# Kernel optimization log

Measured on AMD Instinct MI355X. Metric: run time of the kernel, lower is better.

Reference implementation:

```python
import jax, jax.numpy as jnp
import numpy as np

D_MODEL = 512; N_HEADS = 8; HEAD = D_MODEL // N_HEADS; D_FF = 2048
N_LAYERS = 4; VOCAB = 32000; B = 2; S = 1024; T = 1024


def _posenc(seq_len, d_model):
    pos = np.arange(seq_len)[:, None].astype(np.float32)
    div = np.exp(np.arange(0, d_model, 2).astype(np.float32) * (-np.log(10000.0) / d_model))
    pe = np.zeros((seq_len, d_model), dtype=np.float32)
    pe[:, 0::2] = np.sin(pos * div)
    pe[:, 1::2] = np.cos(pos * div)
    return jnp.asarray(pe)


def _layernorm(x, g, b, eps=1e-6):
    mean = x.mean(-1, keepdims=True)
    xc = x - mean
    # torch .var() is unbiased (ddof=1) -- replicate exactly
    var = (xc * xc).sum(-1, keepdims=True) / (x.shape[-1] - 1)
    return g * (xc * (var + eps) ** -0.5) + b


def _mha(q, k, v, w, mask):
    # w: [4, D, D] stacked (W_q, W_k, W_v, W_o), applied as x @ W
    def heads(x, wi):
        return (x @ wi).reshape(x.shape[0], x.shape[1], N_HEADS, HEAD).transpose(0, 2, 1, 3)
    Q, K, V = heads(q, w[0]), heads(k, w[1]), heads(v, w[2])  # [B,H,S,hd]
    att = jnp.einsum('bhqd,bhkd->bhqk', Q, K) * HEAD ** (-0.5)
    att = jnp.where(mask == 0, -jnp.inf, att)
    att = jax.nn.softmax(att, axis=-1)
    y = jnp.einsum('bhqk,bhkd->bhqd', att, V)
    y = y.transpose(0, 2, 1, 3).reshape(q.shape[0], q.shape[1], D_MODEL)
    return y @ w[3]


def _ff(x, w1, b1, w2, b2):
    return jax.nn.relu(x @ w1 + b1) @ w2 + b2


def setup_inputs() -> dict:
    key = jax.random.key(0)
    ks = iter(jax.random.split(key, 32))
    std = 0.02
    inp = {}
    inp['src'] = jax.random.randint(next(ks), (B, S), 0, VOCAB)
    inp['tgt'] = jax.random.randint(next(ks), (B, T), 0, VOCAB)
    inp['src_mask'] = jnp.ones((B, 1, 1, S), dtype=jnp.int32)
    inp['tgt_mask'] = jnp.tril(jnp.ones((T, T), dtype=jnp.int32))[None, None].repeat(B, axis=0)
    inp['src_emb'] = jax.random.normal(next(ks), (VOCAB, D_MODEL)) * std
    inp['tgt_emb'] = jax.random.normal(next(ks), (VOCAB, D_MODEL)) * std
    inp['enc_att_w'] = jax.random.normal(next(ks), (N_LAYERS, 4, D_MODEL, D_MODEL)) * std
    inp['enc_ff_w1'] = jax.random.normal(next(ks), (N_LAYERS, D_MODEL, D_FF)) * std
    inp['enc_ff_b1'] = jnp.zeros((N_LAYERS, D_FF))
    inp['enc_ff_w2'] = jax.random.normal(next(ks), (N_LAYERS, D_FF, D_MODEL)) * std
    inp['enc_ff_b2'] = jnp.zeros((N_LAYERS, D_MODEL))
    inp['enc_norm_g'] = jnp.ones((N_LAYERS, 2, D_MODEL))
    inp['enc_norm_b'] = jnp.zeros((N_LAYERS, 2, D_MODEL))
    inp['enc_final_g'] = jnp.ones((D_MODEL,))
    inp['enc_final_b'] = jnp.zeros((D_MODEL,))
    inp['dec_att_w'] = jax.random.normal(next(ks), (N_LAYERS, 2, 4, D_MODEL, D_MODEL)) * std
    inp['dec_ff_w1'] = jax.random.normal(next(ks), (N_LAYERS, D_MODEL, D_FF)) * std
    inp['dec_ff_b1'] = jnp.zeros((N_LAYERS, D_FF))
    inp['dec_ff_w2'] = jax.random.normal(next(ks), (N_LAYERS, D_FF, D_MODEL)) * std
    inp['dec_ff_b2'] = jnp.zeros((N_LAYERS, D_MODEL))
    inp['dec_norm_g'] = jnp.ones((N_LAYERS, 3, D_MODEL))
    inp['dec_norm_b'] = jnp.zeros((N_LAYERS, 3, D_MODEL))
    inp['dec_final_g'] = jnp.ones((D_MODEL,))
    inp['dec_final_b'] = jnp.zeros((D_MODEL,))
    inp['proj_w'] = jax.random.normal(next(ks), (D_MODEL, VOCAB)) * std
    inp['proj_b'] = jnp.zeros((VOCAB,))
    return inp


def reference(src, tgt, src_mask, tgt_mask, src_emb, tgt_emb,
              enc_att_w, enc_ff_w1, enc_ff_b1, enc_ff_w2, enc_ff_b2,
              enc_norm_g, enc_norm_b, enc_final_g, enc_final_b,
              dec_att_w, dec_ff_w1, dec_ff_b1, dec_ff_w2, dec_ff_b2,
              dec_norm_g, dec_norm_b, dec_final_g, dec_final_b,
              proj_w, proj_b):
    scale = jnp.float32(np.sqrt(D_MODEL))
    # Encoder (pre-norm residuals: x = x + layer(norm(x)); dropout=0)
    x = src_emb[src] * scale + _posenc(S, D_MODEL)[None]
    for i in range(N_LAYERS):
        z = _layernorm(x, enc_norm_g[i, 0], enc_norm_b[i, 0])
        x = x + _mha(z, z, z, enc_att_w[i], src_mask)
        z = _layernorm(x, enc_norm_g[i, 1], enc_norm_b[i, 1])
        x = x + _ff(z, enc_ff_w1[i], enc_ff_b1[i], enc_ff_w2[i], enc_ff_b2[i])
    enc = _layernorm(x, enc_final_g, enc_final_b)
    # Decoder
    y = tgt_emb[tgt] * scale + _posenc(T, D_MODEL)[None]
    for i in range(N_LAYERS):
        z = _layernorm(y, dec_norm_g[i, 0], dec_norm_b[i, 0])
        y = y + _mha(z, z, z, dec_att_w[i, 0], tgt_mask)
        z = _layernorm(y, dec_norm_g[i, 1], dec_norm_b[i, 1])
        y = y + _mha(z, enc, enc, dec_att_w[i, 1], src_mask)
        z = _layernorm(y, dec_norm_g[i, 2], dec_norm_b[i, 2])
        y = y + _ff(z, dec_ff_w1[i], dec_ff_b1[i], dec_ff_w2[i], dec_ff_b2[i])
    dec = _layernorm(y, dec_final_g, dec_final_b)
    return dec @ proj_w + proj_b  # [B, T, VOCAB] logits
```

## Files before the change

### kernel.cpp

```cpp
#include <hip/hip_runtime.h>
#include <hip/hip_bf16.h>
#include <math.h>

#define D_MODEL 512
#define N_HEADS 8
#define HEAD 64
#define D_FF   2048
#define N_LAYERS 4
#define VOCAB  32000
#define BATCH  2
#define SEQ    1024

typedef __attribute__((ext_vector_type(8))) short bf16x8;
typedef __attribute__((ext_vector_type(4))) float f32x4;

__device__ __forceinline__ float b2f(short s) {
    unsigned int u = ((unsigned int)(unsigned short)s) << 16;
    float f; __builtin_memcpy(&f, &u, 4);
    return f;
}
__device__ __forceinline__ short f2b(float f) {
    __hip_bfloat16 h = __float2bfloat16(f);
    unsigned short u; __builtin_memcpy(&u, &h, 2);
    return (short)u;
}
__device__ __forceinline__ void storev(float* p, float v) { *p = v; }
__device__ __forceinline__ void storev(short* p, float v) { *p = f2b(v); }

__device__ __forceinline__ void transT_tile(const float* __restrict__ s,
                                            short* __restrict__ d,
                                            int K, int N, int tx, int ty, int tid) {
    __shared__ float t[64][65];
    int r = tid >> 2, c4 = (tid & 3) * 4;
#pragma unroll
    for (int jj = 0; jj < 4; ++jj) {
        int col = c4 + jj * 16;
        *(float4*)&t[r][col] = *(const float4*)(s + (size_t)(ty * 64 + r) * N + tx * 64 + col);
    }
    __syncthreads();
#pragma unroll
    for (int jj = 0; jj < 4; ++jj) {
        int kc = c4 + jj * 16;
        short4 o = make_short4(f2b(t[kc][r]), f2b(t[kc + 1][r]),
                               f2b(t[kc + 2][r]), f2b(t[kc + 3][r]));
        *(short4*)(d + (size_t)(tx * 64 + r) * K + ty * 64 + kc) = o;
    }
}

__global__ __launch_bounds__(256) void transT_kernel(const float* __restrict__ src,
                                                     short* __restrict__ dst,
                                                     int K, int N) {
    const float* s = src + (size_t)blockIdx.z * K * N;
    short* d = dst + (size_t)blockIdx.z * K * N;
    transT_tile(s, d, K, N, blockIdx.x, blockIdx.y, threadIdx.x);
}

__global__ __launch_bounds__(256) void repack_attT_kernel(const float* __restrict__ encw,
                                                          const float* __restrict__ decw,
                                                          short* __restrict__ w_enc_qkv,
                                                          short* __restrict__ w_dec_qkv,
                                                          short* __restrict__ w_dec_kv,
                                                          short* __restrict__ w_o) {
    int z = blockIdx.y;
    const float* s; short* d;
    if (z < 12)      { int i = z / 3, j = z % 3;
                       s = encw + (size_t)(i * 4 + j) * 262144;
                       d = w_enc_qkv + (size_t)i * 786432 + j * 262144; }
    else if (z < 24) { int u = z - 12, i = u / 3, j = u % 3;
                       s = decw + (size_t)(i * 8 + j) * 262144;
                       d = w_dec_qkv + (size_t)i * 786432 + j * 262144; }
    else if (z < 32) { int u = z - 24, i = u / 2, j = u % 2;
                       s = decw + (size_t)(i * 8 + 5 + j) * 262144;
                       d = w_dec_kv + (size_t)i * 524288 + j * 262144; }
    else             { int u = z - 32; const float* b; int mi;
                       if (u < 4)       { b = encw; mi = u * 4 + 3; }
                       else if (u < 8)  { b = decw; mi = (u - 4) * 8 + 3; }
                       else if (u < 12) { b = decw; mi = (u - 8) * 8 + 4; }
                       else             { b = decw; mi = (u - 12) * 8 + 7; }
                       s = b + (size_t)mi * 262144; d = w_o + (size_t)u * 262144; }
    int bx = blockIdx.x;
    transT_tile(s, d, 512, 512, bx & 7, bx >> 3, threadIdx.x);
}

__global__ void embed_kernel(const int* __restrict__ tokA, const int* __restrict__ tokB,
                             const float* __restrict__ embA, const float* __restrict__ embB,
                             float* __restrict__ outA, float* __restrict__ outB) {
    int row = blockIdx.x;
    const int* tok = blockIdx.y ? tokB : tokA;
    const float* emb = blockIdx.y ? embB : embA;
    float* out = blockIdx.y ? outB : outA;
    int s = row % SEQ;
    int token = tok[row];
    const float scale = 22.627416997969522f;
    const float c = -1.7988945941359737e-2f;
    for (int d = threadIdx.x; d < D_MODEL; d += blockDim.x) {
        int i2 = (d >> 1) * 2;
        float div = expf((float)i2 * c);
        float ang = (float)s * div;
        float pe = (d & 1) ? cosf(ang) : sinf(ang);
        out[(size_t)row * D_MODEL + d] = emb[(size_t)token * D_MODEL + d] * scale + pe;
    }
}

__global__ __launch_bounds__(256) void ln_kernel(const float* __restrict__ x,
                                                 const float* __restrict__ g,
                                                 const float* __restrict__ b,
                                                 short* __restrict__ out) {
    int row = blockIdx.x * 4 + (threadIdx.x >> 6);
    int lane = threadIdx.x & 63;
    const float4* xr = (const float4*)(x + (size_t)row * D_MODEL);
    float4 v0 = xr[lane * 2], v1 = xr[lane * 2 + 1];
    float c[8] = { v0.x, v0.y, v0.z, v0.w, v1.x, v1.y, v1.z, v1.w };
    float s = ((c[0] + c[1]) + (c[2] + c[3])) + ((c[4] + c[5]) + (c[6] + c[7]));
#pragma unroll
    for (int off = 1; off < 64; off <<= 1) s += __shfl_xor(s, off);
    float mean = s * (1.0f / 512.0f);
    float q = 0.0f;
#pragma unroll
    for (int j = 0; j < 8; ++j) { c[j] -= mean; q += c[j] * c[j]; }
#pragma unroll
    for (int off = 1; off < 64; off <<= 1) q += __shfl_xor(q, off);
    float inv = 1.0f / sqrtf(q * (1.0f / 511.0f) + 1e-6f);
    const float4* gp = (const float4*)g;
    const float4* bp = (const float4*)b;
    float4 g0 = gp[lane * 2], g1 = gp[lane * 2 + 1];
    float4 b0 = bp[lane * 2], b1 = bp[lane * 2 + 1];
    float gg[8] = { g0.x, g0.y, g0.z, g0.w, g1.x, g1.y, g1.z, g1.w };
    float bb[8] = { b0.x, b0.y, b0.z, b0.w, b1.x, b1.y, b1.z, b1.w };
    bf16x8 res;
#pragma unroll
    for (int j = 0; j < 8; ++j) res[j] = f2b(gg[j] * (c[j] * inv) + bb[j]);
    *(bf16x8*)(out + (size_t)row * D_MODEL + lane * 8) = res;
}

__global__ __launch_bounds__(256) void mfma_gemm(const short* __restrict__ A,
                                                 const short* __restrict__ WT,
                                                 const float* bias,
                                                 float* __restrict__ C,
                                                 int M, int N, int K) {
    __shared__ __align__(16) short As[128][40];
    __shared__ __align__(16) short Bs[128][40];
    int tid = threadIdx.x;
    int lane = tid & 63, wid = tid >> 6;
    int wm = wid >> 1, wn = wid & 1;
    int gx = gridDim.x;
    int bid = blockIdx.y * gx + blockIdx.x;
    int per = (gx * gridDim.y) >> 3;
    int nb = (bid & 7) * per + (bid >> 3);
    int brow = (nb % gx) * 128;
    int bcol = (nb / gx) * 128;
    int l15 = lane & 15, lk = lane >> 4;

    f32x4 acc[4][4] = {};

    for (int k0 = 0; k0 < K; k0 += 32) {
#pragma unroll
        for (int j = 0; j < 2; ++j) {
            int c = tid + 256 * j;
            int r = c >> 2, seg = (c & 3) * 8;
            *(bf16x8*)&As[r][seg] = *(const bf16x8*)(A  + (size_t)(brow + r) * K + k0 + seg);
            *(bf16x8*)&Bs[r][seg] = *(const bf16x8*)(WT + (size_t)(bcol + r) * K + k0 + seg);
        }
        __syncthreads();
        bf16x8 af[4], bfv[4];
#pragma unroll
        for (int mf = 0; mf < 4; ++mf)
            af[mf] = *(const bf16x8*)&As[64 * wm + 16 * mf + l15][8 * lk];
#pragma unroll
        for (int nf = 0; nf < 4; ++nf)
            bfv[nf] = *(const bf16x8*)&Bs[64 * wn + 16 * nf + l15][8 * lk];
        __builtin_amdgcn_s_setprio(1);
#pragma unroll
        for (int mf = 0; mf < 4; ++mf)
#pragma unroll
            for (int nf = 0; nf < 4; ++nf)
                acc[mf][nf] = __builtin_amdgcn_mfma_f32_16x16x32_bf16(af[mf], bfv[nf], acc[mf][nf], 0, 0, 0);
        __builtin_amdgcn_s_setprio(0);
        __syncthreads();
    }

#pragma unroll
    for (int mf = 0; mf < 4; ++mf) {
#pragma unroll
        for (int nf = 0; nf < 4; ++nf) {
            int n = bcol + 64 * wn + 16 * nf + l15;
            float bv = bias ? bias[n] : 0.0f;
#pragma unroll
            for (int reg = 0; reg < 4; ++reg) {
                int m = brow + 64 * wm + 16 * mf + lk * 4 + reg;
                __builtin_nontemporal_store(acc[mf][nf][reg] + bv, C + (size_t)m * N + n);
            }
        }
    }
}

template <typename OutT, int ATOMIC>
__global__ __launch_bounds__(256) void mfma_gemm64(const short* __restrict__ A,
                                                   const short* __restrict__ WT,
                                                   const float* bias, const float* resid,
                                                   OutT* __restrict__ C,
                                                   short* __restrict__ vt, int vcol0,
                                                   int M, int N, int K, int relu) {
    __shared__ __align__(16) short As[64][136];
    __shared__ __align__(16) short Bs[64][136];
    int tid = threadIdx.x;
    int lane = tid & 63, wid = tid >> 6;
    int wm = wid >> 1, wn = wid & 1;
    int gx = gridDim.x, gy = gridDim.y;
    int bid = blockIdx.y * gx + blockIdx.x;
    int per = (gx * gy) >> 3;
    int nb = (bid & 7) * per + (bid >> 3);
    int brow = (nb % gy) * 64;
    int bcol = (nb / gy) * 64;
    int l15 = lane & 15, lk = lane >> 4;

    int kz = ATOMIC ? blockIdx.z : 0;
    int kper = ATOMIC ? (K / gridDim.z) : K;
    int kbeg = kz * kper, kend = kbeg + kper;

    f32x4 acc[2][2] = {};

    int ra = tid >> 2, sa = (tid & 3) * 32;

    for (int k0 = kbeg; k0 < kend; k0 += 128) {
        {
            const short* ab = A + (size_t)(brow + ra) * K + k0 + sa;
            const short* wb = WT + (size_t)(bcol + ra) * K + k0 + sa;
#pragma unroll
            for (int j = 0; j < 4; ++j) {
                *(bf16x8*)&As[ra][sa + 8 * j] = *(const bf16x8*)(ab + 8 * j);
                *(bf16x8*)&Bs[ra][sa + 8 * j] = *(const bf16x8*)(wb + 8 * j);
            }
        }
        __syncthreads();
        __builtin_amdgcn_s_setprio(1);
#pragma unroll
        for (int ks = 0; ks < 4; ++ks) {
            bf16x8 a0 = *(const bf16x8*)&As[32 * wm + l15][32 * ks + 8 * lk];
            bf16x8 a1 = *(const bf16x8*)&As[32 * wm + 16 + l15][32 * ks + 8 * lk];
            bf16x8 b0 = *(const bf16x8*)&Bs[32 * wn + l15][32 * ks + 8 * lk];
            bf16x8 b1 = *(const bf16x8*)&Bs[32 * wn + 16 + l15][32 * ks + 8 * lk];
            acc[0][0] = __builtin_amdgcn_mfma_f32_16x16x32_bf16(a0, b0, acc[0][0], 0, 0, 0);
            acc[0][1] = __builtin_amdgcn_mfma_f32_16x16x32_bf16(a0, b1, acc[0][1], 0, 0, 0);
            acc[1][0] = __builtin_amdgcn_mfma_f32_16x16x32_bf16(a1, b0, acc[1][0], 0, 0, 0);
            acc[1][1] = __builtin_amdgcn_mfma_f32_16x16x32_bf16(a1, b1, acc[1][1], 0, 0, 0);
        }
        __builtin_amdgcn_s_setprio(0);
        __syncthreads();
    }

    if constexpr (ATOMIC) {
        float* Cf = (float*)C;
#pragma unroll
        for (int mf = 0; mf < 2; ++mf) {
#pragma unroll
            for (int nf = 0; nf < 2; ++nf) {
                int n = bcol + 32 * wn + 16 * nf + l15;
                float bv = (kz == 0 && bias) ? bias[n] : 0.0f;
#pragma unroll
                for (int reg = 0; reg < 4; ++reg) {
                    int m = brow + 32 * wm + 16 * mf + lk * 4 + reg;
                    atomicAdd(Cf + (size_t)m * N + n, acc[mf][nf][reg] + bv);
                }
            }
        }
        return;
    }

    if (vt && bcol >= vcol0) {
#pragma unroll
        for (int mf = 0; mf < 2; ++mf) {
#pragma unroll
            for (int nf = 0; nf < 2; ++nf) {
                int rel = bcol + 32 * wn + 16 * nf + l15 - vcol0;
                int hh = rel >> 6, dd = rel & 63;
                int m0 = brow + 32 * wm + 16 * mf + 4 * lk;
                int b = m0 >> 10, k = m0 & 1023;
                short4 o4 = make_short4(f2b(acc[mf][nf][0]), f2b(acc[mf][nf][1]),
                                        f2b(acc[mf][nf][2]), f2b(acc[mf][nf][3]));
                *(short4*)(vt + (((size_t)b * N_HEADS + hh) * HEAD + dd) * SEQ + k) = o4;
            }
        }
        return;
    }

#pragma unroll
    for (int mf = 0; mf < 2; ++mf) {
#pragma unroll
        for (int nf = 0; nf < 2; ++nf) {
            int n = bcol + 32 * wn + 16 * nf + l15;
            float bv = bias ? bias[n] : 0.0f;
#pragma unroll
            for (int reg = 0; reg < 4; ++reg) {
                int m = brow + 32 * wm + 16 * mf + lk * 4 + reg;
                float v = acc[mf][nf][reg] + bv;
                if (resid) v += resid[(size_t)m * N + n];
                if (relu)  v = fmaxf(v, 0.0f);
                storev(C + (size_t)m * N + n, v);
            }
        }
    }
}

__global__ __launch_bounds__(128) void fattn_kernel(const short* __restrict__ Q, int strq,
                                                    const short* __restrict__ Kp, int strkv,
                                                    const short* __restrict__ Vtg,
                                                    short* __restrict__ out, int causal) {
    __shared__ __align__(16) short Ks[64][72];
    __shared__ __align__(16) short Vs[64][72];
    __shared__ __align__(16) short Ps[32][72];
    int tid = threadIdx.x;
    int lane = tid & 63, w = tid >> 6;
    int l15 = lane & 15, lk = lane >> 4;
    int qt = blockIdx.x, h = blockIdx.y, bb = blockIdx.z;
    int q0 = qt * 32;

    bf16x8 qf[2];
    {
        const short* qbase = Q + ((size_t)(bb * SEQ + q0 + 16 * w + l15)) * strq + h * HEAD;
        qf[0] = *(const bf16x8*)(qbase + 8 * lk);
        qf[1] = *(const bf16x8*)(qbase + 32 + 8 * lk);
    }

    f32x4 o[4] = {};
    float lsum = 0.0f;

    int nkt = causal ? ((q0 + 31) / 64 + 1) : (SEQ / 64);
    int rr = tid >> 1, sg = (tid & 1) * 32;
    int qg = q0 + 16 * w + l15;

    const short* vbase = Vtg + (((size_t)bb * N_HEADS + h) * HEAD + rr) * SEQ;

    for (int ktile = 0; ktile < nkt; ++ktile) {
        int k0 = ktile * 64;
        __syncthreads();
        {
            const short* ksrc = Kp + ((size_t)(bb * SEQ + k0 + rr)) * strkv + h * HEAD + sg;
            const short* vsrc = vbase + k0 + sg;
#pragma unroll
            for (int j = 0; j < 4; ++j) {
                *(bf16x8*)&Ks[rr][sg + 8 * j] = *(const bf16x8*)(ksrc + 8 * j);
                *(bf16x8*)&Vs[rr][sg + 8 * j] = *(const bf16x8*)(vsrc + 8 * j);
            }
        }
        __syncthreads();

        f32x4 s[4] = {};
        __builtin_amdgcn_s_setprio(1);
#pragma unroll
        for (int kf = 0; kf < 4; ++kf) {
            bf16x8 k0f = *(const bf16x8*)&Ks[16 * kf + l15][8 * lk];
            bf16x8 k1f = *(const bf16x8*)&Ks[16 * kf + l15][32 + 8 * lk];
            s[kf] = __builtin_amdgcn_mfma_f32_16x16x32_bf16(k0f, qf[0], s[kf], 0, 0, 0);
            s[kf] = __builtin_amdgcn_mfma_f32_16x16x32_bf16(k1f, qf[1], s[kf], 0, 0, 0);
        }
        __builtin_amdgcn_s_setprio(0);

        bool diag = causal && (ktile == nkt - 1);
        float psum = 0.0f;
#pragma unroll
        for (int kf = 0; kf < 4; ++kf) {
            short4 pq;
#pragma unroll
            for (int r = 0; r < 4; ++r) {
                float sv = s[kf][r] * 0.125f;
                if (diag && (k0 + 16 * kf + 4 * lk + r > qg)) sv = -1e30f;
                float p = __expf(sv);
                psum += p;
                ((short*)&pq)[r] = f2b(p);
            }
            *(short4*)&Ps[16 * w + l15][16 * kf + 4 * lk] = pq;
        }
        psum += __shfl_xor(psum, 16);
        psum += __shfl_xor(psum, 32);
        lsum += psum;

        __builtin_amdgcn_s_setprio(1);
#pragma unroll
        for (int ks = 0; ks < 2; ++ks) {
            bf16x8 pb = *(const bf16x8*)&Ps[16 * w + l15][32 * ks + 8 * lk];
#pragma unroll
            for (int df = 0; df < 4; ++df) {
                bf16x8 vf = *(const bf16x8*)&Vs[16 * df + l15][32 * ks + 8 * lk];
                o[df] = __builtin_amdgcn_mfma_f32_16x16x32_bf16(vf, pb, o[df], 0, 0, 0);
            }
        }
        __builtin_amdgcn_s_setprio(0);
    }

    float inv = 1.0f / lsum;
    short* orow = out + ((size_t)(bb * SEQ + qg)) * D_MODEL + h * HEAD;
#pragma unroll
    for (int df = 0; df < 4; ++df) {
        short4 o4 = make_short4(f2b(o[df][0] * inv), f2b(o[df][1] * inv),
                                f2b(o[df][2] * inv), f2b(o[df][3] * inv));
        *(short4*)(orow + 16 * df + 4 * lk) = o4;
    }
}

extern "C" void kernel_launch(void* const* d_in, const int* in_sizes, int n_in,
                              void* d_out, int out_size, void* d_ws, size_t ws_size,
                              hipStream_t stream) {
    const int*   src       = (const int*)  d_in[0];
    const int*   tgt       = (const int*)  d_in[1];
    const float* src_emb   = (const float*)d_in[4];
    const float* tgt_emb   = (const float*)d_in[5];
    const float* enc_att_w = (const float*)d_in[6];
    const float* enc_ff_w1 = (const float*)d_in[7];
    const float* enc_ff_b1 = (const float*)d_in[8];
    const float* enc_ff_w2 = (const float*)d_in[9];
    const float* enc_ff_b2 = (const float*)d_in[10];
    const float* enc_norm_g= (const float*)d_in[11];
    const float* enc_norm_b= (const float*)d_in[12];
    const float* enc_fin_g = (const float*)d_in[13];
    const float* enc_fin_b = (const float*)d_in[14];
    const float* dec_att_w = (const float*)d_in[15];
    const float* dec_ff_w1 = (const float*)d_in[16];
    const float* dec_ff_b1 = (const float*)d_in[17];
    const float* dec_ff_w2 = (const float*)d_in[18];
    const float* dec_ff_b2 = (const float*)d_in[19];
    const float* dec_norm_g= (const float*)d_in[20];
    const float* dec_norm_b= (const float*)d_in[21];
    const float* dec_fin_g = (const float*)d_in[22];
    const float* dec_fin_b = (const float*)d_in[23];
    const float* proj_w    = (const float*)d_in[24];
    const float* proj_b    = (const float*)d_in[25];
    float* out = (float*)d_out;

    const int NROW = BATCH * SEQ;
    const size_t CH = (size_t)NROW * D_MODEL;
    float* ws = (float*)d_ws;
    float* x = ws;
    float* y = x + CH;
    short* z    = (short*)(y + CH);
    short* qkv  = z + CH;
    short* ab   = qkv + 3 * CH;
    short* encb = ab + CH;
    short* ff   = encb + CH;
    short* vt   = ff + 4 * CH;
    short* wts  = vt + CH;

    short* w_enc_qkv = wts;
    short* w_dec_qkv = w_enc_qkv + 4 * 786432;
    short* w_dec_kv  = w_dec_qkv + 4 * 786432;
    short* w_o       = w_dec_kv  + 4 * 524288;
    short* w_enc_ff1 = w_o       + 16 * 262144;
    short* w_enc_ff2 = w_enc_ff1 + 4194304;
    short* w_dec_ff1 = w_enc_ff2 + 4194304;
    short* w_dec_ff2 = w_dec_ff1 + 4194304;
    short* w_proj    = w_dec_ff2 + 4194304;

    {
        dim3 ga(64, 48);
        repack_attT_kernel<<<ga, 256, 0, stream>>>(enc_att_w, dec_att_w,
                                                   w_enc_qkv, w_dec_qkv, w_dec_kv, w_o);
        dim3 gf1(D_FF / 64, D_MODEL / 64, 4);
        transT_kernel<<<gf1, 256, 0, stream>>>(enc_ff_w1, w_enc_ff1, D_MODEL, D_FF);
        transT_kernel<<<gf1, 256, 0, stream>>>(dec_ff_w1, w_dec_ff1, D_MODEL, D_FF);
        dim3 gf2(D_MODEL / 64, D_FF / 64, 4);
        transT_kernel<<<gf2, 256, 0, stream>>>(enc_ff_w2, w_enc_ff2, D_FF, D_MODEL);
        transT_kernel<<<gf2, 256, 0, stream>>>(dec_ff_w2, w_dec_ff2, D_FF, D_MODEL);
        dim3 gp(VOCAB / 64, D_MODEL / 64);
        transT_kernel<<<gp, 256, 0, stream>>>(proj_w, w_proj, D_MODEL, VOCAB);
    }

    auto g64_b = [&](const short* A, const short* W, const float* bias, const float* resid,
                     short* C, short* vto, int vcol0, int M, int N, int K, int relu) {
        dim3 g(N / 64, M / 64);
        mfma_gemm64<short, 0><<<g, 256, 0, stream>>>(A, W, bias, resid, C, vto, vcol0, M, N, K, relu);
    };
    auto g64_atomic = [&](const short* A, const short* W, const float* bias,
                          float* C, int M, int N, int K, int split) {
        dim3 g(N / 64, M / 64, split);
        mfma_gemm64<float, 1><<<g, 256, 0, stream>>>(A, W, bias, nullptr, C, nullptr, 0, M, N, K, 0);
    };
    auto ln = [&](const float* in, const float* g, const float* b, short* outp) {
        ln_kernel<<<NROW / 4, 256, 0, stream>>>(in, g, b, outp);
    };
    auto attn = [&](const short* Q, int strq, const short* K, int strkv, short* O, int causal) {
        dim3 g(SEQ / 32, N_HEADS, BATCH);
        fattn_kernel<<<g, 128, 0, stream>>>(Q, strq, K, strkv, vt, O, causal);
    };

    {
        dim3 ge(NROW, 2);
        embed_kernel<<<ge, 256, 0, stream>>>(src, tgt, src_emb, tgt_emb, x, y);
    }

    for (int i = 0; i < N_LAYERS; ++i) {
        ln(x, enc_norm_g + (i * 2 + 0) * D_MODEL, enc_norm_b + (i * 2 + 0) * D_MODEL, z);
        g64_b(z, w_enc_qkv + (size_t)i * 786432, nullptr, nullptr, qkv, vt, 1024, NROW, 1536, D_MODEL, 0);
        attn(qkv, 1536, qkv + 512, 1536, ab, 0);
        g64_atomic(ab, w_o + (size_t)i * 262144, nullptr, x, NROW, D_MODEL, D_MODEL, 2);
        ln(x, enc_norm_g + (i * 2 + 1) * D_MODEL, enc_norm_b + (i * 2 + 1) * D_MODEL, z);
        g64_b(z, w_enc_ff1 + (size_t)i * 1048576, enc_ff_b1 + i * D_FF, nullptr, ff, nullptr, 0, NROW, D_FF, D_MODEL, 1);
        g64_atomic(ff, w_enc_ff2 + (size_t)i * 1048576, enc_ff_b2 + i * D_MODEL, x, NROW, D_MODEL, D_FF, 4);
    }
    ln(x, enc_fin_g, enc_fin_b, encb);

    for (int i = 0; i < N_LAYERS; ++i) {
        ln(y, dec_norm_g + (i * 3 + 0) * D_MODEL, dec_norm_b + (i * 3 + 0) * D_MODEL, z);
        g64_b(z, w_dec_qkv + (size_t)i * 786432, nullptr, nullptr, qkv, vt, 1024, NROW, 1536, D_MODEL, 0);
        attn(qkv, 1536, qkv + 512, 1536, ab, 1);
        g64_atomic(ab, w_o + (size_t)(4 + i) * 262144, nullptr, y, NROW, D_MODEL, D_MODEL, 2);
        {
            short* crossq = qkv;
            short* kv     = qkv + CH;
            ln(y, dec_norm_g + (i * 3 + 1) * D_MODEL, dec_norm_b + (i * 3 + 1) * D_MODEL, z);
            g64_b(z, w_o + (size_t)(8 + i) * 262144, nullptr, nullptr, crossq, nullptr, 0, NROW, D_MODEL, D_MODEL, 0);
            g64_b(encb, w_dec_kv + (size_t)i * 524288, nullptr, nullptr, kv, vt, 512, NROW, 1024, D_MODEL, 0);
            attn(crossq, 512, kv, 1024, ab, 0);
        }
        g64_atomic(ab, w_o + (size_t)(12 + i) * 262144, nullptr, y, NROW, D_MODEL, D_MODEL, 2);
        ln(y, dec_norm_g + (i * 3 + 2) * D_MODEL, dec_norm_b + (i * 3 + 2) * D_MODEL, z);
        g64_b(z, w_dec_ff1 + (size_t)i * 1048576, dec_ff_b1 + i * D_FF, nullptr, ff, nullptr, 0, NROW, D_FF, D_MODEL, 1);
        g64_atomic(ff, w_dec_ff2 + (size_t)i * 1048576, dec_ff_b2 + i * D_MODEL, y, NROW, D_MODEL, D_FF, 4);
    }
    ln(y, dec_fin_g, dec_fin_b, z);

    dim3 pg(NROW / 128, VOCAB / 128);
    mfma_gemm<<<pg, 256, 0, stream>>>(z, w_proj, proj_b, out, NROW, VOCAB, D_MODEL);
}
```

Baseline: 1.111 ms.

## Split attention key tiles across two wave pairs and reduce partial outputs

The flash attention kernel now runs 256 threads per block. Two groups of two waves each process half of the key tiles for the same 32 queries, then combine their partial outputs and row sums through shared memory. This halves the serial key loop per block and raises the wave count, which targets latency in attention. The cost is a shared-memory reduction at the end, more LDS per block, and idle waves on the odd causal tile.

```diff
diff --git a/kernel.cpp b/kernel.cpp
--- a/kernel.cpp
+++ b/kernel.cpp
@@ -302,22 +302,31 @@
     }
 }
 
-__global__ __launch_bounds__(128) void fattn_kernel(const short* __restrict__ Q, int strq,
+__global__ __launch_bounds__(256) void fattn_kernel(const short* __restrict__ Q, int strq,
                                                     const short* __restrict__ Kp, int strkv,
                                                     const short* __restrict__ Vtg,
                                                     short* __restrict__ out, int causal) {
-    __shared__ __align__(16) short Ks[64][72];
-    __shared__ __align__(16) short Vs[64][72];
-    __shared__ __align__(16) short Ps[32][72];
+    __shared__ __align__(16) short smem[23040];
+    short* KsB = smem;
+    short* VsB = smem + 9216;
+    short* PsB = smem + 18432;
+    float* red = (float*)smem;
+
     int tid = threadIdx.x;
     int lane = tid & 63, w = tid >> 6;
     int l15 = lane & 15, lk = lane >> 4;
+    int qsub = w & 1, khalf = w >> 1;
+    int t127 = tid & 127;
     int qt = blockIdx.x, h = blockIdx.y, bb = blockIdx.z;
     int q0 = qt * 32;
 
+    short* Ks = KsB + khalf * 4608;
+    short* Vs = VsB + khalf * 4608;
+    short* Ps = PsB + khalf * 2304;
+
     bf16x8 qf[2];
     {
-        const short* qbase = Q + ((size_t)(bb * SEQ + q0 + 16 * w + l15)) * strq + h * HEAD;
+        const short* qbase = Q + ((size_t)(bb * SEQ + q0 + 16 * qsub + l15)) * strq + h * HEAD;
         qf[0] = *(const bf16x8*)(qbase + 8 * lk);
         qf[1] = *(const bf16x8*)(qbase + 32 + 8 * lk);
     }
@@ -326,37 +335,42 @@
     float lsum = 0.0f;
 
     int nkt = causal ? ((q0 + 31) / 64 + 1) : (SEQ / 64);
-    int rr = tid >> 1, sg = (tid & 1) * 32;
-    int qg = q0 + 16 * w + l15;
+    int half0 = (nkt + 1) >> 1, half1 = nkt - half0;
+
+    int rr = t127 >> 1, sg = (t127 & 1) * 32;
+    int qg = q0 + 16 * qsub + l15;
 
     const short* vbase = Vtg + (((size_t)bb * N_HEADS + h) * HEAD + rr) * SEQ;
 
-    for (int ktile = 0; ktile < nkt; ++ktile) {
-        int k0 = ktile * 64;
+    for (int t = 0; t < half0; ++t) {
+        int myTile = khalf ? (half0 + t) : t;
+        bool active = khalf ? (t < half1) : true;
+        int k0 = myTile * 64;
         __syncthreads();
-        {
+        if (active) {
             const short* ksrc = Kp + ((size_t)(bb * SEQ + k0 + rr)) * strkv + h * HEAD + sg;
             const short* vsrc = vbase + k0 + sg;
 #pragma unroll
             for (int j = 0; j < 4; ++j) {
-                *(bf16x8*)&Ks[rr][sg + 8 * j] = *(const bf16x8*)(ksrc + 8 * j);
-                *(bf16x8*)&Vs[rr][sg + 8 * j] = *(const bf16x8*)(vsrc + 8 * j);
+                *(bf16x8*)&Ks[rr * 72 + sg + 8 * j] = *(const bf16x8*)(ksrc + 8 * j);
+                *(bf16x8*)&Vs[rr * 72 + sg + 8 * j] = *(const bf16x8*)(vsrc + 8 * j);
             }
         }
         __syncthreads();
+        if (!active) continue;
 
         f32x4 s[4] = {};
         __builtin_amdgcn_s_setprio(1);
 #pragma unroll
         for (int kf = 0; kf < 4; ++kf) {
-            bf16x8 k0f = *(const bf16x8*)&Ks[16 * kf + l15][8 * lk];
-            bf16x8 k1f = *(const bf16x8*)&Ks[16 * kf + l15][32 + 8 * lk];
+            bf16x8 k0f = *(const bf16x8*)&Ks[(16 * kf + l15) * 72 + 8 * lk];
+            bf16x8 k1f = *(const bf16x8*)&Ks[(16 * kf + l15) * 72 + 32 + 8 * lk];
             s[kf] = __builtin_amdgcn_mfma_f32_16x16x32_bf16(k0f, qf[0], s[kf], 0, 0, 0);
             s[kf] = __builtin_amdgcn_mfma_f32_16x16x32_bf16(k1f, qf[1], s[kf], 0, 0, 0);
         }
         __builtin_amdgcn_s_setprio(0);
 
-        bool diag = causal && (ktile == nkt - 1);
+        bool diag = causal && (myTile == nkt - 1);
         float psum = 0.0f;
 #pragma unroll
         for (int kf = 0; kf < 4; ++kf) {
@@ -369,7 +383,7 @@
                 psum += p;
                 ((short*)&pq)[r] = f2b(p);
             }
-            *(short4*)&Ps[16 * w + l15][16 * kf + 4 * lk] = pq;
+            *(short4*)&Ps[(16 * qsub + l15) * 72 + 16 * kf + 4 * lk] = pq;
         }
         psum += __shfl_xor(psum, 16);
         psum += __shfl_xor(psum, 32);
@@ -378,23 +392,38 @@
         __builtin_amdgcn_s_setprio(1);
 #pragma unroll
         for (int ks = 0; ks < 2; ++ks) {
-            bf16x8 pb = *(const bf16x8*)&Ps[16 * w + l15][32 * ks + 8 * lk];
+            bf16x8 pb = *(const bf16x8*)&Ps[(16 * qsub + l15) * 72 + 32 * ks + 8 * lk];
 #pragma unroll
             for (int df = 0; df < 4; ++df) {
-                bf16x8 vf = *(const bf16x8*)&Vs[16 * df + l15][32 * ks + 8 * lk];
+                bf16x8 vf = *(const bf16x8*)&Vs[(16 * df + l15) * 72 + 32 * ks + 8 * lk];
                 o[df] = __builtin_amdgcn_mfma_f32_16x16x32_bf16(vf, pb, o[df], 0, 0, 0);
             }
         }
         __builtin_amdgcn_s_setprio(0);
     }
 
-    float inv = 1.0f / lsum;
-    short* orow = out + ((size_t)(bb * SEQ + qg)) * D_MODEL + h * HEAD;
-#pragma unroll
-    for (int df = 0; df < 4; ++df) {
-        short4 o4 = make_short4(f2b(o[df][0] * inv), f2b(o[df][1] * inv),
-                                f2b(o[df][2] * inv), f2b(o[df][3] * inv));
-        *(short4*)(orow + 16 * df + 4 * lk) = o4;
+    __syncthreads();
+    {
+        int base = (w * 64 + lane) * 17;
+#pragma unroll
+        for (int df = 0; df < 4; ++df)
+#pragma unroll
+            for (int r = 0; r < 4; ++r) red[base + df * 4 + r] = o[df][r];
+        red[base + 16] = lsum;
+    }
+    __syncthreads();
+    if (khalf == 0) {
+        int pbase = ((w + 2) * 64 + lane) * 17;
+        float inv = 1.0f / (lsum + red[pbase + 16]);
+        short* orow = out + ((size_t)(bb * SEQ + qg)) * D_MODEL + h * HEAD;
+#pragma unroll
+        for (int df = 0; df < 4; ++df) {
+            short4 o4 = make_short4(f2b((o[df][0] + red[pbase + df * 4 + 0]) * inv),
+                                    f2b((o[df][1] + red[pbase + df * 4 + 1]) * inv),
+                                    f2b((o[df][2] + red[pbase + df * 4 + 2]) * inv),
+                                    f2b((o[df][3] + red[pbase + df * 4 + 3]) * inv));
+            *(short4*)(orow + 16 * df + 4 * lk) = o4;
+        }
     }
 }
 
@@ -479,7 +508,7 @@
     };
     auto attn = [&](const short* Q, int strq, const short* K, int strkv, short* O, int causal) {
         dim3 g(SEQ / 32, N_HEADS, BATCH);
-        fattn_kernel<<<g, 128, 0, stream>>>(Q, strq, K, strkv, vt, O, causal);
+        fattn_kernel<<<g, 256, 0, stream>>>(Q, strq, K, strkv, vt, O, causal);
     };
 
     {
```

Result: faster. 1.051 ms (-5.4%).
